# Optimization experiments

Hardware: AMD Instinct MI355X
Metric: run time of the kernel (lower is better)

## Reference

```python
import jax, jax.numpy as jnp
import numpy as np

H = 90            # hidden_size (hard-coded in module)
NODE_F = 16       # conv1 in_channels = dim(x) + dim(pos)
EDGE_F = 8
N_GRAPHS = 512


def _init_linear(key, fan_in, fan_out):
    kw, kb = jax.random.split(key)
    bound = 1.0 / np.sqrt(fan_in)
    w = jax.random.uniform(kw, (fan_in, fan_out), minval=-bound, maxval=bound, dtype=jnp.float32)
    b = jax.random.uniform(kb, (fan_out,), minval=-bound, maxval=bound, dtype=jnp.float32)
    return w, b


def setup_inputs() -> dict:
    key = jax.random.key(0)
    ks = jax.random.split(key, 16)
    N, E = 16000, 64000
    x = jax.random.normal(ks[0], (N, 13), dtype=jnp.float32)
    pos = jax.random.normal(ks[1], (N, 3), dtype=jnp.float32)
    edge_attr = jax.random.normal(ks[2], (E, EDGE_F), dtype=jnp.float32)
    edge_index = jax.random.randint(ks[3], (2, E), 0, N, dtype=jnp.int32)
    batch = jnp.sort(jax.random.randint(ks[4], (N,), 0, N_GRAPHS, dtype=jnp.int32))

    # conv1: edge MLP edge_f -> H -> NODE_F*H ; root [NODE_F,H]; bias [H]
    c1_w1, c1_b1 = _init_linear(ks[5], EDGE_F, H)
    c1_w2, c1_b2 = _init_linear(ks[6], H, NODE_F * H)
    c1_root = jax.random.normal(ks[7], (NODE_F, H), dtype=jnp.float32) / np.sqrt(NODE_F)
    c1_bias = jnp.zeros((H,), dtype=jnp.float32)
    # conv2: H -> H
    c2_w1, c2_b1 = _init_linear(ks[8], EDGE_F, H)
    c2_w2, c2_b2 = _init_linear(ks[9], H, H * H)
    c2_root = jax.random.normal(ks[10], (H, H), dtype=jnp.float32) / np.sqrt(H)
    c2_bias = jnp.zeros((H,), dtype=jnp.float32)
    # conv3: H -> H//2
    c3_w1, c3_b1 = _init_linear(ks[11], EDGE_F, H)
    c3_w2, c3_b2 = _init_linear(ks[12], H, H * (H // 2))
    c3_root = jax.random.normal(ks[13], (H, H // 2), dtype=jnp.float32) / np.sqrt(H)
    c3_bias = jnp.zeros((H // 2,), dtype=jnp.float32)

    fc1_w, fc1_b = _init_linear(ks[14], H // 2, H)
    out_w, out_b = _init_linear(ks[15], H, 1)

    return dict(x=x, pos=pos, edge_attr=edge_attr, edge_index=edge_index, batch=batch,
                c1_w1=c1_w1, c1_b1=c1_b1, c1_w2=c1_w2, c1_b2=c1_b2, c1_root=c1_root, c1_bias=c1_bias,
                c2_w1=c2_w1, c2_b1=c2_b1, c2_w2=c2_w2, c2_b2=c2_b2, c2_root=c2_root, c2_bias=c2_bias,
                c3_w1=c3_w1, c3_b1=c3_b1, c3_w2=c3_w2, c3_b2=c3_b2, c3_root=c3_root, c3_bias=c3_bias,
                fc1_w=fc1_w, fc1_b=fc1_b, out_w=out_w, out_b=out_b)


def _nnconv(x, src, dst, edge_attr, w1, b1, w2, b2, root, bias, in_c, out_c):
    # edge MLP -> per-edge weight matrix theta[e] in R^{in_c x out_c}
    h = jax.nn.relu(edge_attr @ w1 + b1)                  # [E, H]
    theta = (h @ w2 + b2).reshape(-1, in_c, out_c)        # [E, in_c, out_c]
    msg = jnp.einsum('ei,eio->eo', x[src], theta)         # gather + per-edge matvec
    agg = jax.ops.segment_sum(msg, dst, num_segments=x.shape[0])  # scatter-add
    return agg + x @ root + bias


def reference(x, pos, edge_attr, edge_index, batch,
              c1_w1, c1_b1, c1_w2, c1_b2, c1_root, c1_bias,
              c2_w1, c2_b1, c2_w2, c2_b2, c2_root, c2_bias,
              c3_w1, c3_b1, c3_w2, c3_b2, c3_root, c3_bias,
              fc1_w, fc1_b, out_w, out_b):
    src, dst = edge_index[0], edge_index[1]
    h = jnp.concatenate([x, pos], axis=1)                 # [N, NODE_F]
    h = jax.nn.relu(_nnconv(h, src, dst, edge_attr, c1_w1, c1_b1, c1_w2, c1_b2, c1_root, c1_bias, NODE_F, H))
    h = jax.nn.relu(_nnconv(h, src, dst, edge_attr, c2_w1, c2_b1, c2_w2, c2_b2, c2_root, c2_bias, H, H))
    h = jax.nn.relu(_nnconv(h, src, dst, edge_attr, c3_w1, c3_b1, c3_w2, c3_b2, c3_root, c3_bias, H, H // 2))
    g = jax.ops.segment_sum(h, batch, num_segments=N_GRAPHS)  # global_add_pool
    g = jax.nn.relu(g @ fc1_w + fc1_b)
    return g @ out_w + out_b                               # [N_GRAPHS, 1]
```

## Files before the change

kernel.cpp:

```cpp
#include <hip/hip_runtime.h>

#define NN 16000
#define NE 64000
#define HD 90
#define NG 512

typedef float f32x4 __attribute__((ext_vector_type(4)));
typedef short s16x8 __attribute__((ext_vector_type(8)));

__device__ __forceinline__ unsigned short rhu1(float f) {
  return (unsigned short)((__builtin_bit_cast(unsigned int, f) + 0x8000u) >> 16);
}
__device__ __forceinline__ unsigned int rhu_pack(float lo, float hi) {
  unsigned int ul = __builtin_bit_cast(unsigned int, lo) + 0x8000u;
  unsigned int uh = __builtin_bit_cast(unsigned int, hi) + 0x8000u;
  return __builtin_amdgcn_perm(uh, ul, 0x07060302u);
}
__device__ __forceinline__ float bfhi(unsigned int u) {
  return __builtin_bit_cast(float, u & 0xFFFF0000u);
}
__device__ __forceinline__ float bflo(unsigned int u) {
  return __builtin_bit_cast(float, u << 16);
}

__global__ void concat_kernel(const float* __restrict__ x, const float* __restrict__ pos,
                              float* __restrict__ h0) {
  int idx = blockIdx.x * 256 + threadIdx.x;
  if (idx >= NN * 16) return;
  int n = idx >> 4, c = idx & 15;
  h0[idx] = (c < 13) ? x[n * 13 + c] : pos[n * 3 + (c - 13)];
}

__global__ void edge_mlp_bf(const float* __restrict__ ea, const float* __restrict__ w1,
                            const float* __restrict__ b1, unsigned short* __restrict__ he) {
  int idx = blockIdx.x * 256 + threadIdx.x;
  if (idx >= NE * 96) return;
  int e = idx / 96, k = idx - e * 96;
  unsigned short v;
  if (k < 90) {
    const float* a = ea + e * 8;
    float acc = b1[k];
#pragma unroll
    for (int j = 0; j < 8; j++) acc = fmaf(a[j], w1[j * HD + k], acc);
    v = rhu1(fmaxf(acc, 0.f));
  } else {
    v = (k == 90) ? (unsigned short)0x3F80 : (unsigned short)0;
  }
  he[idx] = v;
}

template <int OC, int NTT>
__global__ void wprep_frag(const float* __restrict__ w2, const float* __restrict__ b2,
                           unsigned short* __restrict__ wout, int inc_oc) {
  const int i = blockIdx.x / 3, c = blockIdx.x - 3 * (blockIdx.x / 3);
  __shared__ float t_s[32 * 100];
  const int tid = threadIdx.x;
  for (int idx = tid; idx < 32 * 96; idx += 256) {
    int kk = idx / 96, o = idx - kk * 96;
    int hk = c * 32 + kk;
    float v = 0.f;
    if (o < OC) {
      if (hk < 90) v = w2[hk * inc_oc + i * OC + o];
      else if (hk == 90) v = b2[i * OC + o];
    }
    t_s[kk * 100 + o] = v;
  }
  __syncthreads();
  unsigned int* wo = (unsigned int*)(wout + (size_t)i * NTT * 3 * 512) + c * 256;
  for (int idx = tid; idx < NTT * 256; idx += 256) {
    int t = idx >> 8, r = idx & 255;
    int lane = r >> 2, u = r & 3;
    int kk = (lane >> 4) * 8 + 2 * u;
    int o = t * 16 + (lane & 15);
    wo[(size_t)t * 3 * 256 + lane * 4 + u] = rhu_pack(t_s[kk * 100 + o], t_s[(kk + 1) * 100 + o]);
  }
}

template <int ILIM, int OC, int NTT, int NWG, int MT, int EPB, int BLK>
__global__ __launch_bounds__(BLK, 2)
void msg_mfma(const unsigned short* __restrict__ he,
              const float* __restrict__ nin,
              const int* __restrict__ src, const int* __restrict__ dst,
              const unsigned short* __restrict__ wp,
              float* __restrict__ agg) {
  constexpr int WMG = EPB / 32;
  constexpr int TPE = BLK / EPB;
  constexpr int NWAVES = BLK / 64;
  constexpr int NF = NTT * 3;
  constexpr int MG = MT / 2;
  __shared__ unsigned short zb[ILIM * WMG * 32];
  __shared__ unsigned short wbA[NF * 512];
  __shared__ unsigned short wbB[NF * 512];
  __shared__ int dst_s[EPB];
  const int tid = threadIdx.x;
  const int e0 = blockIdx.x * EPB;
  const int wid = tid >> 6, l = tid & 63, ln = tid & 15, q = (tid & 63) >> 4;
  const int wn = wid % NWG, wm = wid / NWG;
  const int eb = wm * MT * 16;
  const int wn3 = wn * 3;

  const unsigned short* wl = wp + l * 8;
  auto stage = [&](const unsigned short* wb, unsigned short* lb) {
#pragma unroll
    for (int t = 0; t < (NF + NWAVES - 1) / NWAVES; t++) {
      const int s = wid + t * NWAVES;
      if (s < NF) {
        __builtin_amdgcn_global_load_lds(
            (const __attribute__((address_space(1))) unsigned int*)(wb + (size_t)s * 512),
            (__attribute__((address_space(3))) unsigned int*)(lb + s * 512),
            16, 0, 0);
      }
    }
  };

  f32x4 acc[MT][3];
  s16x8 af[MT][3];
  auto compute = [&](int i, const unsigned short* lb) {
    f32x4 zv[MT];
#pragma unroll
    for (int g = 0; g < MG; g++) {
      const uint4 zu = *(const uint4*)&zb[(i * WMG + wm * MG + g) * 32 + q * 8];
      zv[2 * g][0] = bflo(zu.x); zv[2 * g][1] = bfhi(zu.x);
      zv[2 * g][2] = bflo(zu.y); zv[2 * g][3] = bfhi(zu.y);
      zv[2 * g + 1][0] = bflo(zu.z); zv[2 * g + 1][1] = bfhi(zu.z);
      zv[2 * g + 1][2] = bflo(zu.w); zv[2 * g + 1][3] = bfhi(zu.w);
    }
    uint4 ba[9];
#pragma unroll
    for (int ntl = 0; ntl < 3; ntl++)
#pragma unroll
      for (int c = 0; c < 3; c++)
        ba[ntl * 3 + c] = *(const uint4*)(lb + ((wn3 + ntl) * 3 + c) * 512 + l * 8);
#pragma unroll
    for (int ntl = 0; ntl < 3; ntl++) {
#pragma unroll
      for (int mt = 0; mt < MT; mt++) {
        f32x4 t = __builtin_amdgcn_mfma_f32_16x16x32_bf16(af[mt][0], __builtin_bit_cast(s16x8, ba[ntl * 3 + 0]), (f32x4)0.f, 0, 0, 0);
        t = __builtin_amdgcn_mfma_f32_16x16x32_bf16(af[mt][1], __builtin_bit_cast(s16x8, ba[ntl * 3 + 1]), t, 0, 0, 0);
        t = __builtin_amdgcn_mfma_f32_16x16x32_bf16(af[mt][2], __builtin_bit_cast(s16x8, ba[ntl * 3 + 2]), t, 0, 0, 0);
        acc[mt][ntl] += zv[mt] * t;
      }
    }
  };

  stage(wl, wbA);

  if (tid < EPB) dst_s[tid] = dst[e0 + tid];

  {
    const int e = tid % EPB, jj = tid / EPB;
    const int base = (e >> 5) * 32 + (((e & 15) >> 2) << 3) + (((e >> 4) & 1) << 2) + (e & 3);
    const float* zr = nin + (size_t)src[e0 + e] * ILIM;
    for (int p = jj; p < ILIM / 2; p += TPE) {
      const float2 v = *(const float2*)(zr + 2 * p);
      zb[(2 * p) * (WMG * 32) + base] = rhu1(v.x);
      zb[(2 * p + 1) * (WMG * 32) + base] = rhu1(v.y);
    }
  }

#pragma unroll
  for (int mt = 0; mt < MT; mt++) {
    const unsigned short* hr = he + (size_t)(e0 + eb + mt * 16 + ln) * 96 + q * 8;
#pragma unroll
    for (int c = 0; c < 3; c++) af[mt][c] = *(const s16x8*)(hr + c * 32);
  }

#pragma unroll
  for (int mt = 0; mt < MT; mt++)
#pragma unroll
    for (int nt = 0; nt < 3; nt++) acc[mt][nt] = (f32x4)0.f;

  __syncthreads();

  const unsigned short* wnext = wl + (size_t)NF * 512;

#pragma clang loop unroll(disable)
  for (int i = 0; i < ILIM; i += 2) {
    stage(wnext, wbB);
    wnext += (size_t)NF * 512;
    compute(i, wbA);
    __syncthreads();
    if (i + 2 < ILIM) {
      stage(wnext, wbA);
      wnext += (size_t)NF * 512;
    }
    compute(i + 1, wbB);
    if (i + 2 < ILIM) __syncthreads();
  }

#pragma unroll
  for (int mt = 0; mt < MT; mt++) {
#pragma unroll
    for (int ntl = 0; ntl < 3; ntl++) {
      int o = wn * 48 + ntl * 16 + ln;
      if (o < OC) {
#pragma unroll
        for (int r = 0; r < 4; r++) {
          int el = eb + mt * 16 + q * 4 + r;
          atomicAdd(agg + (size_t)dst_s[el] * OC + o, acc[mt][ntl][r]);
        }
      }
    }
  }
}

template <int IN_C, int OC>
__global__ void node_kernel(const float* __restrict__ agg, const float* __restrict__ nin,
                            const float* __restrict__ root, const float* __restrict__ bias,
                            float* __restrict__ out) {
  int idx = blockIdx.x * 256 + threadIdx.x;
  if (idx >= NN * OC) return;
  int n = idx / OC, o = idx - n * OC;
  float acc = agg[idx] + bias[o];
  const float* inp = nin + (size_t)n * IN_C;
#pragma unroll 6
  for (int i = 0; i < IN_C; i++) acc = fmaf(inp[i], root[i * OC + o], acc);
  out[idx] = fmaxf(acc, 0.f);
}

__global__ void pool_mlp_kernel(const float* __restrict__ h3, const int* __restrict__ batch,
                                const float* __restrict__ fc1_w, const float* __restrict__ fc1_b,
                                const float* __restrict__ out_w, const float* __restrict__ out_b,
                                float* __restrict__ out) {
  const int b = blockIdx.x;
  const int tid = threadIdx.x;
  __shared__ float g[45];
  __shared__ float go[90];
  __shared__ int rng[2];
  if (tid < 2) {
    int target = b + tid;
    int lo = 0, hi = NN;
    while (lo < hi) { int mid = (lo + hi) >> 1; if (batch[mid] < target) lo = mid + 1; else hi = mid; }
    rng[tid] = lo;
  }
  __syncthreads();
  const int s = rng[0], e = rng[1];
  if (tid < 45) {
    float acc = 0.f;
    for (int n = s; n < e; n++) acc += h3[n * 45 + tid];
    g[tid] = acc;
  }
  __syncthreads();
  if (tid < 90) {
    float acc = fc1_b[tid];
#pragma unroll 5
    for (int i = 0; i < 45; i++) acc = fmaf(g[i], fc1_w[i * 90 + tid], acc);
    go[tid] = fmaxf(acc, 0.f) * out_w[tid];
  }
  __syncthreads();
  if (tid == 0) {
    float acc = out_b[0];
    for (int i = 0; i < 90; i++) acc += go[i];
    out[b] = acc;
  }
}

extern "C" void kernel_launch(void* const* d_in, const int* in_sizes, int n_in,
                              void* d_out, int out_size, void* d_ws, size_t ws_size,
                              hipStream_t stream) {
  const float* x       = (const float*)d_in[0];
  const float* pos     = (const float*)d_in[1];
  const float* ea      = (const float*)d_in[2];
  const int*   eidx    = (const int*)d_in[3];
  const int*   batch   = (const int*)d_in[4];
  const float* c1_w1   = (const float*)d_in[5];
  const float* c1_b1   = (const float*)d_in[6];
  const float* c1_w2   = (const float*)d_in[7];
  const float* c1_b2   = (const float*)d_in[8];
  const float* c1_root = (const float*)d_in[9];
  const float* c1_bias = (const float*)d_in[10];
  const float* c2_w1   = (const float*)d_in[11];
  const float* c2_b1   = (const float*)d_in[12];
  const float* c2_w2   = (const float*)d_in[13];
  const float* c2_b2   = (const float*)d_in[14];
  const float* c2_root = (const float*)d_in[15];
  const float* c2_bias = (const float*)d_in[16];
  const float* c3_w1   = (const float*)d_in[17];
  const float* c3_b1   = (const float*)d_in[18];
  const float* c3_w2   = (const float*)d_in[19];
  const float* c3_b2   = (const float*)d_in[20];
  const float* c3_root = (const float*)d_in[21];
  const float* c3_bias = (const float*)d_in[22];
  const float* fc1_w   = (const float*)d_in[23];
  const float* fc1_b   = (const float*)d_in[24];
  const float* out_w   = (const float*)d_in[25];
  const float* out_b   = (const float*)d_in[26];
  const int* src = eidx;
  const int* dst = eidx + NE;

  float* ws  = (float*)d_ws;
  float* h0  = ws;
  float* h1  = h0 + NN * 16;
  float* h2  = h1 + NN * 90;
  float* h3  = h2 + NN * 90;
  float* agg = h3 + NN * 45;
  unsigned short* he_bf = (unsigned short*)(agg + NN * 90);
  unsigned short* wp1 = he_bf + (size_t)NE * 96;
  unsigned short* wp2 = wp1 + (size_t)16 * 6 * 3 * 512;
  unsigned short* wp3 = wp2 + (size_t)90 * 6 * 3 * 512;

  concat_kernel<<<(NN * 16) / 256, 256, 0, stream>>>(x, pos, h0);

  wprep_frag<90, 6><<<16 * 3, 256, 0, stream>>>(c1_w2, c1_b2, wp1, 16 * 90);
  wprep_frag<90, 6><<<90 * 3, 256, 0, stream>>>(c2_w2, c2_b2, wp2, 90 * 90);
  wprep_frag<45, 3><<<90 * 3, 256, 0, stream>>>(c3_w2, c3_b2, wp3, 90 * 45);

  hipMemsetAsync(agg, 0, (size_t)NN * 90 * sizeof(float), stream);
  edge_mlp_bf<<<(NE * 96) / 256, 256, 0, stream>>>(ea, c1_w1, c1_b1, he_bf);
  msg_mfma<16, 90, 6, 2, 4, 128, 256><<<NE / 128, 256, 0, stream>>>(he_bf, h0, src, dst, wp1, agg);
  node_kernel<16, 90><<<(NN * 90) / 256, 256, 0, stream>>>(agg, h0, c1_root, c1_bias, h1);

  hipMemsetAsync(agg, 0, (size_t)NN * 90 * sizeof(float), stream);
  edge_mlp_bf<<<(NE * 96) / 256, 256, 0, stream>>>(ea, c2_w1, c2_b1, he_bf);
  msg_mfma<90, 90, 6, 2, 4, 128, 256><<<NE / 128, 256, 0, stream>>>(he_bf, h1, src, dst, wp2, agg);
  node_kernel<90, 90><<<(NN * 90) / 256, 256, 0, stream>>>(agg, h1, c2_root, c2_bias, h2);

  hipMemsetAsync(agg, 0, (size_t)NN * 45 * sizeof(float), stream);
  edge_mlp_bf<<<(NE * 96) / 256, 256, 0, stream>>>(ea, c3_w1, c3_b1, he_bf);
  msg_mfma<90, 45, 3, 1, 4, 128, 128><<<NE / 128, 128, 0, stream>>>(he_bf, h2, src, dst, wp3, agg);
  node_kernel<90, 45><<<(NN * 45 + 255) / 256, 256, 0, stream>>>(agg, h2, c3_root, c3_bias, h3);

  pool_mlp_kernel<<<NG, 128, 0, stream>>>(h3, batch, fc1_w, fc1_b, out_w, out_b, (float*)d_out);
}
```

Measured before the change: 541.9 us.

## Triple-buffer weight staging with partial vmcnt waits in message kernel

Replaces the double-buffered LDS weight staging with a three-buffer ring that prefetches two slices ahead. Each step now waits with an explicit partial s_waitcnt vmcnt plus a raw s_barrier instead of __syncthreads, so the newest prefetch can stay in flight across the barrier. This should hide more of the global-to-LDS latency. The cost is an extra LDS buffer, which may reduce occupancy, and hardcoded vmcnt immediates that depend on how many loads each wave issues.

```diff
diff --git a/kernel.cpp b/kernel.cpp
--- a/kernel.cpp
+++ b/kernel.cpp
@@ -88,9 +88,13 @@
   constexpr int NWAVES = BLK / 64;
   constexpr int NF = NTT * 3;
   constexpr int MG = MT / 2;
+  constexpr int FLO = NF / NWAVES;
+  constexpr int FHI = FLO + ((NF % NWAVES) ? 1 : 0);
+  static_assert(FLO == 4 && FHI == 5, "vmcnt immediates hardcoded for 5/4");
   __shared__ unsigned short zb[ILIM * WMG * 32];
-  __shared__ unsigned short wbA[NF * 512];
-  __shared__ unsigned short wbB[NF * 512];
+  __shared__ unsigned short wb0[NF * 512];
+  __shared__ unsigned short wb1[NF * 512];
+  __shared__ unsigned short wb2[NF * 512];
   __shared__ int dst_s[EPB];
   const int tid = threadIdx.x;
   const int e0 = blockIdx.x * EPB;
@@ -98,19 +102,29 @@
   const int wn = wid % NWG, wm = wid / NWG;
   const int eb = wm * MT * 16;
   const int wn3 = wn * 3;
+  const bool hiw = wid < (NF % NWAVES);
 
   const unsigned short* wl = wp + l * 8;
-  auto stage = [&](const unsigned short* wb, unsigned short* lb) {
+  auto stage = [&](int ii, unsigned short* lb) {
 #pragma unroll
     for (int t = 0; t < (NF + NWAVES - 1) / NWAVES; t++) {
       const int s = wid + t * NWAVES;
       if (s < NF) {
         __builtin_amdgcn_global_load_lds(
-            (const __attribute__((address_space(1))) unsigned int*)(wb + (size_t)s * 512),
+            (const __attribute__((address_space(1))) unsigned int*)(wl + ((size_t)ii * NF + s) * 512),
             (__attribute__((address_space(3))) unsigned int*)(lb + s * 512),
             16, 0, 0);
       }
     }
+  };
+
+  auto vmw = [&]() {
+    if (hiw) asm volatile("s_waitcnt vmcnt(5)" ::: "memory");
+    else     asm volatile("s_waitcnt vmcnt(4)" ::: "memory");
+  };
+  auto barrier = [&]() {
+    __builtin_amdgcn_s_barrier();
+    __builtin_amdgcn_sched_barrier(0);
   };
 
   f32x4 acc[MT][3];
@@ -143,7 +157,8 @@
     }
   };
 
-  stage(wl, wbA);
+  stage(0, wb0);
+  stage(1, wb1);
 
   if (tid < EPB) dst_s[tid] = dst[e0 + tid];
 
@@ -172,20 +187,33 @@
 
   __syncthreads();
 
-  const unsigned short* wnext = wl + (size_t)NF * 512;
-
+  constexpr int NMAIN = (ILIM >= 5) ? ((ILIM - 5) / 3 + 1) : 0;
 #pragma clang loop unroll(disable)
-  for (int i = 0; i < ILIM; i += 2) {
-    stage(wnext, wbB);
-    wnext += (size_t)NF * 512;
-    compute(i, wbA);
-    __syncthreads();
+  for (int g = 0; g < NMAIN; ++g) {
+    const int i0 = 3 * g;
+    stage(i0 + 2, wb2);
+    compute(i0, wb0);
+    vmw(); barrier();
+    stage(i0 + 3, wb0);
+    compute(i0 + 1, wb1);
+    vmw(); barrier();
+    stage(i0 + 4, wb1);
+    compute(i0 + 2, wb2);
+    vmw(); barrier();
+  }
+
+#pragma clang loop unroll(disable)
+  for (int i = 3 * NMAIN; i < ILIM; ++i) {
     if (i + 2 < ILIM) {
-      stage(wnext, wbA);
-      wnext += (size_t)NF * 512;
-    }
-    compute(i + 1, wbB);
-    if (i + 2 < ILIM) __syncthreads();
+      const int r = (i + 2) % 3;
+      stage(i + 2, r == 0 ? wb0 : (r == 1 ? wb1 : wb2));
+    }
+    {
+      const int r = i % 3;
+      compute(i, r == 0 ? wb0 : (r == 1 ? wb1 : wb2));
+    }
+    asm volatile("s_waitcnt vmcnt(0)" ::: "memory");
+    barrier();
   }
 
 #pragma unroll
```

Result: slower. 748.8 us (+38.2%).
